# Optimization experiments

Hardware: AMD Instinct MI355X
Metric: run time of the kernel (lower is better)

Reference implementation:

```python
import jax, jax.numpy as jnp
import numpy as np

B = 4096
N = 8192
LEVEL_SIZES = [8, 128, 2048, 6008]  # sums to N; 4-level taxonomy
EPS = 1e-07


def _build_hierarchy():
    """parent[c] = parent node index (-1 for roots); level_of[c] = depth."""
    rng = np.random.default_rng(0)
    parent = np.full(N, -1, np.int32)
    level_of = np.zeros(N, np.int32)
    off, prev_start, prev_size = 0, 0, 0
    for l, sz in enumerate(LEVEL_SIZES):
        level_of[off:off + sz] = l
        if l > 0:
            parent[off:off + sz] = rng.integers(prev_start, prev_start + prev_size, sz)
        prev_start, prev_size = off, sz
        off += sz
    return parent, level_of


def setup_inputs() -> dict:
    key = jax.random.key(0)
    k1, k2 = jax.random.split(key)
    pred = jax.random.normal(k1, (B, N), dtype=jnp.float32)  # logits
    target = (jax.random.uniform(k2, (B, N)) < 0.02).astype(jnp.float32)
    parent_np, level_np = _build_hierarchy()
    return {
        "pred": pred,
        "target": target,
        "parent": jnp.asarray(parent_np),
        "level_of": jnp.asarray(level_np),
        "mode": 0,  # 0 = EVAL (propagate conditional probs), 1 = TRAIN
    }


def reference(pred, target, parent, level_of, mode):
    p = jax.nn.sigmoid(pred)                      # [B, N]
    parent_clip = jnp.maximum(parent, 0)          # safe gather index for roots
    is_root = parent < 0                          # recursive_relation[-1]

    if mode != 1:  # not 'TRAIN': top-down conditional probability propagation
        pc = p
        for l in range(1, len(LEVEL_SIZES)):
            # pred_clone[:, children(n)] = pred[:, children] * pred_clone[:, n]
            pc = jnp.where(level_of == l, p * pc[:, parent_clip], pc)
        pred_clone = pc
    else:
        pred_clone = None

    # mask[b, c] = 1 if c is a root, or if target[b, parent[c]] == 1
    mask = jnp.where(is_root, jnp.float32(1.0), target[:, parent_clip])

    pcl = jnp.clip(p, EPS, 1.0 - EPS)
    loss = -(jnp.log(pcl) * target + (1.0 - target) * mask * jnp.log(1.0 - pcl))
    loss = loss.sum(axis=1).mean()
    return (loss, pred_clone)
```

## Files before the change

### kernel.cpp

```cpp
#include <hip/hip_runtime.h>


typedef float f4 __attribute__((ext_vector_type(4)));
typedef float f2 __attribute__((ext_vector_type(2)));
typedef int   i4 __attribute__((ext_vector_type(4)));

#define N_NODES 8192
#define L1S 8
#define L2S 136
#define L3S 2184
#define N4   2048
#define L3S4 546

__device__ __forceinline__ float frcp(float x) { return __builtin_amdgcn_rcpf(x); }

__global__ __launch_bounds__(256, 6) void cs_main(
    const float* __restrict__ pred,
    const float* __restrict__ target,
    const int* __restrict__ parent,
    float* __restrict__ out,
    float* __restrict__ bsum,
    float inv_b)
{
    __shared__ float pk[L3S];

    const int tid = threadIdx.x;
    const int lane = tid & 63;
    const int b = blockIdx.x;
    const float* __restrict__ prow = pred + (size_t)b * N_NODES;
    const float* __restrict__ trow = target + (size_t)b * N_NODES;
    float* __restrict__ obase = out + (size_t)b * N_NODES;
    const f4* __restrict__ Pp = (const f4*)prow;
    const f4* __restrict__ Tp = (const f4*)trow;
    const i4* __restrict__ Qp = (const i4*)parent;

    f4 ax[3];
    {
        f4 at[3];
#pragma unroll
        for (int k = 0; k < 3; ++k) {
            const int g = min(tid + k * 256, L3S4 - 1);
            ax[k] = Pp[g]; at[k] = Tp[g];
        }
#pragma unroll
        for (int k = 0; k < 3; ++k) {
            const int g = tid + k * 256;
            if (g < L3S4) {
                f4 v;
#pragma unroll
                for (int j = 0; j < 4; ++j) {
                    const float p = frcp(1.0f + __expf(-ax[k][j]));
                    v[j] = at[k][j] > 0.5f ? -p : p;
                }
                *(f4*)(pk + 4 * g) = v;
            }
        }
    }
    __syncthreads();

    float lsum = 0.0f;

#pragma unroll
    for (int k = 0; k < 3; ++k) {
        const int g = tid + k * 256;
        if (g < L3S4) {
            const f4 v = *(const f4*)(pk + 4 * g);
            const i4 q = Qp[g];
            f4 cums;
#pragma unroll
            for (int j = 0; j < 4; ++j) {
                const float p = fabsf(v[j]);
                const float tf = (v[j] < 0.0f) ? 1.0f : 0.0f;
                float mf, cum;
                if (g < L1S / 4) {
                    mf = 1.0f; cum = p;
                } else if (g < L2S / 4) {
                    const float pv = pk[q[j]];
                    mf = (pv < 0.0f) ? 1.0f : 0.0f;
                    cum = p * fabsf(pv);
                } else {
                    const float pv = pk[q[j]];
                    const float gv = pk[parent[q[j]]];
                    mf = (pv < 0.0f) ? 1.0f : 0.0f;
                    cum = p * fabsf(pv) * fabsf(gv);
                    pk[4 * g + j] = (tf > 0.0f) ? -cum : cum;
                }
                const float s = -__logf(p);
                const float cx = mf - tf * mf;
                lsum += (tf + cx) * s + cx * ax[k][j];
                cums[j] = cum;
            }
            const float prev3 = __shfl_up(cums[3], 1);
            float* slot = obase + 4 * g;
            if (lane > 0) {
                *(f4*)slot = f4{prev3, cums[0], cums[1], cums[2]};
            } else {
                slot[1] = cums[0];
                *(f2*)(slot + 2) = f2{cums[1], cums[2]};
            }
            if (lane == 63 || g == L3S4 - 1) slot[4] = cums[3];
        }
    }
    __syncthreads();

    int g = L3S4 + tid;
    f4 xA = Pp[g], tA = Tp[g]; i4 qA = Qp[g];
    {
        const int g1 = g + 256;
        f4 xB = Pp[g1], tB = Tp[g1]; i4 qB = Qp[g1];
#pragma unroll
        for (int k = 0; k < 6; ++k) {
            f4 nx, nt; i4 nq;
            if (k < 4) {
                const int gp = min(g + 512, N4 - 1);
                nx = Pp[gp]; nt = Tp[gp]; nq = Qp[gp];
            }
            if (g < N4) {
                f4 rr;
#pragma unroll
                for (int j = 0; j < 4; ++j) {
                    const float x = xA[j], tf = tA[j];
                    const float pv = pk[qA[j]];
                    const float mf = (pv < 0.0f) ? 1.0f : 0.0f;
                    const float e = __expf(-x);
                    const float s = __logf(1.0f + e);
                    const float p = frcp(1.0f + e);
                    const float cx = mf - tf * mf;
                    lsum += (tf + cx) * s + cx * x;
                    rr[j] = p * fabsf(pv);
                }
                const float prev3 = __shfl_up(rr[3], 1);
                float* slot = obase + 4 * g;
                if (lane > 0) {
                    *(f4*)slot = f4{prev3, rr[0], rr[1], rr[2]};
                } else {
                    slot[1] = rr[0];
                    *(f2*)(slot + 2) = f2{rr[1], rr[2]};
                }
                if (lane == 63 || g == N4 - 1) slot[4] = rr[3];
            }
            xA = xB; tA = tB; qA = qB;
            xB = nx; tB = nt; qB = nq;
            g += 256;
        }
    }

#pragma unroll
    for (int off = 32; off > 0; off >>= 1) lsum += __shfl_down(lsum, off);
    if (lane == 0) {
        if (bsum) bsum[b * 4 + (tid >> 6)] = lsum;
        else atomicAdd(out, lsum * inv_b);
    }
}

__global__ __launch_bounds__(256) void cs_finish(
    const float* __restrict__ bsum, float* __restrict__ out,
    int n4, float inv_b)
{
    __shared__ float red[4];
    const int tid = threadIdx.x;
    float s = 0.0f;
    for (int i = tid; i < n4; i += 256) {
        const f4 v = ((const f4*)bsum)[i];
        s += (v[0] + v[1]) + (v[2] + v[3]);
    }
#pragma unroll
    for (int off = 32; off > 0; off >>= 1) s += __shfl_down(s, off);
    if ((tid & 63) == 0) red[tid >> 6] = s;
    __syncthreads();
    if (tid == 0) out[0] = ((red[0] + red[1]) + (red[2] + red[3])) * inv_b;
}

extern "C" void kernel_launch(void* const* d_in, const int* in_sizes, int n_in,
                              void* d_out, int out_size, void* d_ws, size_t ws_size,
                              hipStream_t stream) {
    const float* pred   = (const float*)d_in[0];
    const float* target = (const float*)d_in[1];
    const int*   parent = (const int*)d_in[2];

    float* out = (float*)d_out;
    const int batch = in_sizes[0] / N_NODES;
    const float inv_b = 1.0f / (float)batch;

    if (ws_size >= (size_t)batch * 4 * sizeof(float)) {
        float* bsum = (float*)d_ws;
        cs_main<<<batch, 256, 0, stream>>>(pred, target, parent, out, bsum, inv_b);
        cs_finish<<<1, 256, 0, stream>>>(bsum, out, batch, inv_b);
    } else {
        hipMemsetAsync(d_out, 0, sizeof(float), stream);
        cs_main<<<batch, 256, 0, stream>>>(pred, target, parent, out, nullptr, inv_b);
    }
}
```

Measured before the change: 89.40 us.

## Stream leaf-level pred/target through LDS ring via async global_load_lds

Replaces the register double-buffered loads for the last level with direct global-to-LDS async loads into a two-slot ring, gated by explicit vmcnt waits and sched barriers. The goal is to keep more memory requests in flight and free registers for occupancy. The output store drops the shuffle-based aligned f4 write in favour of unaligned scalar/f2/scalar stores. In exchange it adds 16 KB of LDS per block, which may cap occupancy, and relies on hand-counted vmcnt values. There is no barrier between reusing a ring slot and reading it, which is safe only because each thread reads data its own wave loaded.

```diff
diff --git a/kernel.cpp b/kernel.cpp
--- a/kernel.cpp
+++ b/kernel.cpp
@@ -1,4 +1,5 @@
 #include <hip/hip_runtime.h>
+#include <stdint.h>
 
 
 typedef float f4 __attribute__((ext_vector_type(4)));
@@ -11,8 +12,15 @@
 #define L3S 2184
 #define N4   2048
 #define L3S4 546
+#define NCH 6
 
 __device__ __forceinline__ float frcp(float x) { return __builtin_amdgcn_rcpf(x); }
+
+__device__ __forceinline__ void glds16(const float* g, float* l) {
+    __builtin_amdgcn_global_load_lds(
+        (const __attribute__((address_space(1))) void*)g,
+        (__attribute__((address_space(3))) void*)l, 16, 0, 0);
+}
 
 __global__ __launch_bounds__(256, 6) void cs_main(
     const float* __restrict__ pred,
@@ -23,9 +31,11 @@
     float inv_b)
 {
     __shared__ float pk[L3S];
+    __shared__ float ring[2][2][1024];
 
     const int tid = threadIdx.x;
     const int lane = tid & 63;
+    const int wid = tid >> 6;
     const int b = blockIdx.x;
     const float* __restrict__ prow = pred + (size_t)b * N_NODES;
     const float* __restrict__ trow = target + (size_t)b * N_NODES;
@@ -103,52 +113,61 @@
     }
     __syncthreads();
 
-    int g = L3S4 + tid;
-    f4 xA = Pp[g], tA = Tp[g]; i4 qA = Qp[g];
-    {
-        const int g1 = g + 256;
-        f4 xB = Pp[g1], tB = Tp[g1]; i4 qB = Qp[g1];
-#pragma unroll
-        for (int k = 0; k < 6; ++k) {
-            f4 nx, nt; i4 nq;
-            if (k < 4) {
-                const int gp = min(g + 512, N4 - 1);
-                nx = Pp[gp]; nt = Tp[gp]; nq = Qp[gp];
-            }
-            if (g < N4) {
-                f4 rr;
-#pragma unroll
-                for (int j = 0; j < 4; ++j) {
-                    const float x = xA[j], tf = tA[j];
-                    const float pv = pk[qA[j]];
-                    const float mf = (pv < 0.0f) ? 1.0f : 0.0f;
-                    const float e = __expf(-x);
-                    const float s = __logf(1.0f + e);
-                    const float p = frcp(1.0f + e);
-                    const float cx = mf - tf * mf;
-                    lsum += (tf + cx) * s + cx * x;
-                    rr[j] = p * fabsf(pv);
-                }
-                const float prev3 = __shfl_up(rr[3], 1);
-                float* slot = obase + 4 * g;
-                if (lane > 0) {
-                    *(f4*)slot = f4{prev3, rr[0], rr[1], rr[2]};
-                } else {
-                    slot[1] = rr[0];
-                    *(f2*)(slot + 2) = f2{rr[1], rr[2]};
-                }
-                if (lane == 63 || g == N4 - 1) slot[4] = rr[3];
-            }
-            xA = xB; tA = tB; qA = qB;
-            xB = nx; tB = nt; qB = nq;
-            g += 256;
-        }
-    }
+#define ISSUE(k) do {                                                        \
+        const int gi = min(L3S4 + (k) * 256 + wid * 64 + lane, N4 - 1);      \
+        glds16((const float*)(Pp + gi), &ring[(k) & 1][0][wid * 256]);       \
+        glds16((const float*)(Tp + gi), &ring[(k) & 1][1][wid * 256]);       \
+    } while (0)
+
+    i4 qreg0, qreg1;
+    ISSUE(0);
+    qreg0 = Qp[min(L3S4 + tid, N4 - 1)];
+    ISSUE(1);
+    qreg1 = Qp[min(L3S4 + 256 + tid, N4 - 1)];
+
+#pragma unroll
+    for (int k = 0; k < NCH; ++k) {
+        __builtin_amdgcn_sched_barrier(0);
+        asm volatile("s_waitcnt vmcnt(3)" ::: "memory");
+        __builtin_amdgcn_sched_barrier(0);
+        const int g = L3S4 + k * 256 + tid;
+        if (g < N4) {
+            const f4 x4 = *(const f4*)&ring[k & 1][0][tid * 4];
+            const f4 t4 = *(const f4*)&ring[k & 1][1][tid * 4];
+            const i4 q4 = (k & 1) ? qreg1 : qreg0;
+            f4 rr;
+#pragma unroll
+            for (int j = 0; j < 4; ++j) {
+                const float x = x4[j], tf = t4[j];
+                const float pv = pk[q4[j]];
+                const float mf = (pv < 0.0f) ? 1.0f : 0.0f;
+                const float e = __expf(-x);
+                const float s = __logf(1.0f + e);
+                const float p = frcp(1.0f + e);
+                const float cx = mf - tf * mf;
+                lsum += (tf + cx) * s + cx * x;
+                rr[j] = p * fabsf(pv);
+            }
+            float* slot = obase + 1 + 4 * g;
+            slot[0] = rr[0];
+            *(f2*)(slot + 1) = f2{rr[1], rr[2]};
+            slot[3] = rr[3];
+        }
+        __builtin_amdgcn_sched_barrier(0);
+        if (k + 2 < NCH) {
+            ISSUE(k + 2);
+            if ((k & 1) == 0)
+                qreg0 = Qp[min(L3S4 + (k + 2) * 256 + tid, N4 - 1)];
+            else
+                qreg1 = Qp[min(L3S4 + (k + 2) * 256 + tid, N4 - 1)];
+        }
+    }
+#undef ISSUE
 
 #pragma unroll
     for (int off = 32; off > 0; off >>= 1) lsum += __shfl_down(lsum, off);
     if (lane == 0) {
-        if (bsum) bsum[b * 4 + (tid >> 6)] = lsum;
+        if (bsum) bsum[b * 4 + wid] = lsum;
         else atomicAdd(out, lsum * inv_b);
     }
 }
```

Result: slower. 92.25 us (+3.2%).
